# Performance work log

Measured on AMD Instinct MI355X. Metric: run time of the kernel, lower is better.

The kernel has to match this reference:

```python
import jax, jax.numpy as jnp
import numpy as np
import math

B = 50        # graphs per batch
NPG = 2000    # nodes per graph
EPG = 12000   # edges per graph
F_IN = 256
NHID = 128
RATIO = 0.8


def setup_inputs() -> dict:
    key = jax.random.key(0)
    ks = jax.random.split(key, 12)
    N = B * NPG
    src_loc = jax.random.randint(ks[0], (B, EPG), 0, NPG)
    dst_loc = jax.random.randint(ks[1], (B, EPG), 0, NPG)
    off = (jnp.arange(B) * NPG)[:, None]
    edge_index = jnp.stack([(src_loc + off).reshape(-1), (dst_loc + off).reshape(-1)]).astype(jnp.int32)

    def lin(k, fi, fo):
        return (jax.random.normal(k, (fi, fo), jnp.float32) / np.sqrt(fi).astype(np.float32))

    return {
        "x": jax.random.normal(ks[2], (N, F_IN), jnp.float32),
        "W1": lin(ks[3], F_IN, NHID), "b1": jnp.zeros(NHID, jnp.float32),
        "Ws1": lin(ks[4], NHID, 1), "bs1": jnp.zeros(1, jnp.float32),
        "W2": lin(ks[5], NHID, NHID), "b2": jnp.zeros(NHID, jnp.float32),
        "Ws2": lin(ks[6], NHID, 1), "bs2": jnp.zeros(1, jnp.float32),
        "W3": lin(ks[7], NHID, NHID), "b3": jnp.zeros(NHID, jnp.float32),
        "Ws3": lin(ks[8], NHID, 1), "bs3": jnp.zeros(1, jnp.float32),
        "Wl": lin(ks[9], 2 * NHID, NHID), "bl": jnp.zeros(NHID, jnp.float32),
        "edge_index": edge_index,
    }


def gcn_conv(x, W, b, src, dst, w, N):
    # PyG GCNConv: D^{-1/2} (A + I) D^{-1/2} X W + b, deg from edge weights + self loop
    h = x @ W
    deg = jax.ops.segment_sum(w, dst, num_segments=N) + 1.0
    dis = jax.lax.rsqrt(deg)
    norm = w * dis[src] * dis[dst]                       # [E]
    agg = jax.ops.segment_sum(h[src] * norm[:, None], dst, num_segments=N)
    return agg + h / deg[:, None] + b                    # self-loop norm = 1/deg


def sag_pool(x, src, dst, w, Ws, bs, n_per_graph):
    N = x.shape[0]
    k = math.ceil(RATIO * n_per_graph)
    score = gcn_conv(x, Ws, bs, src, dst, w, N)[:, 0]    # [N]
    _, topi = jax.lax.top_k(score.reshape(B, n_per_graph), k)
    perm = (topi + (jnp.arange(B) * n_per_graph)[:, None]).reshape(-1)
    x_new = x[perm] * jnp.tanh(score[perm])[:, None]
    # filter_adj: keep edges whose endpoints survive, reindex; dropped edges -> weight 0
    mapping = jnp.full((N,), -1, jnp.int32).at[perm].set(jnp.arange(B * k, dtype=jnp.int32))
    ns, nd = mapping[src], mapping[dst]
    valid = (ns >= 0) & (nd >= 0) & (w > 0)
    return (x_new, jnp.where(valid, ns, 0), jnp.where(valid, nd, 0),
            jnp.where(valid, w, jnp.zeros((), x.dtype)), k)


def readout(x, n):
    # global max pool || global mean pool (equal-size graphs, nodes grouped per graph)
    xr = x.reshape(B, n, -1)
    return jnp.concatenate([xr.max(axis=1), xr.mean(axis=1)], axis=-1)


def reference(x, W1, b1, Ws1, bs1, W2, b2, Ws2, bs2, W3, b3, Ws3, bs3, Wl, bl, edge_index):
    src, dst = edge_index[0], edge_index[1]
    w = jnp.ones(src.shape[0], x.dtype)
    n = NPG
    x = jax.nn.relu(gcn_conv(x, W1, b1, src, dst, w, B * n))
    x, src, dst, w, n = sag_pool(x, src, dst, w, Ws1, bs1, n)
    x1 = readout(x, n)
    x = jax.nn.relu(gcn_conv(x, W2, b2, src, dst, w, B * n))
    x, src, dst, w, n = sag_pool(x, src, dst, w, Ws2, bs2, n)
    x2 = readout(x, n)
    x = jax.nn.relu(gcn_conv(x, W3, b3, src, dst, w, B * n))
    x, src, dst, w, n = sag_pool(x, src, dst, w, Ws3, bs3, n)
    x3 = readout(x, n)
    return jax.nn.relu((x1 + x2 + x3) @ Wl + bl)
```

## Files before the change

### kernel.cpp

```cpp
#include <hip/hip_runtime.h>
#include <math.h>

#define B_GRAPHS 50
#define NPG0     2000
#define EPG      12000
#define F_IN_C   256
#define NHID     128
#define N0       (B_GRAPHS * NPG0)
#define NE       (B_GRAPHS * EPG)
#define RSEG     32
#define GSLOTS   7
#define CPAD     136
#define KMAX     1600

typedef _Float16 f16x8 __attribute__((ext_vector_type(8)));
typedef float    f32x4 __attribute__((ext_vector_type(4)));

static inline int cdiv(int a, int b) { return (a + b - 1) / b; }

__global__ void k_fill_start(int* __restrict__ cnt, float* __restrict__ accum) {
    int i = blockIdx.x * 256 + threadIdx.x;
    if (i < N0) cnt[i] = 0;
    if (i < B_GRAPHS * 256) accum[i] = 0.f;
}

__global__ void k_init_cvt(const int* __restrict__ ei, int* __restrict__ esrc,
                           int* __restrict__ edst, float* __restrict__ ew,
                           int* __restrict__ cnt,
                           const float* __restrict__ W1, const float* __restrict__ W2,
                           const float* __restrict__ W3, _Float16* __restrict__ WT1,
                           _Float16* __restrict__ WT2, _Float16* __restrict__ WT3) {
    int t = blockIdx.x * 256 + threadIdx.x;
    if (t < NE) {
        int d = ei[NE + t];
        esrc[t] = ei[t]; edst[t] = d; ew[t] = 1.0f;
        atomicAdd(&cnt[d], 1);
    }
    if (t < 128 * 256) {
        int n = t >> 8, kk = t & 255;
        WT1[t] = (_Float16)W1[kk * 128 + n];
    } else if (t < 128 * 256 + 128 * 128) {
        int u = t - 32768; int n = u >> 7, kk = u & 127;
        WT2[u] = (_Float16)W2[kk * 128 + n];
    } else if (t < 128 * 256 + 2 * 128 * 128) {
        int u = t - 49152; int n = u >> 7, kk = u & 127;
        WT3[u] = (_Float16)W3[kk * 128 + n];
    }
}

template<int FP32IN, int F, int GATHER>
__global__ __launch_bounds__(256) void k_gemm_ws(const void* __restrict__ Xin,
                                                 const _Float16* __restrict__ WT,
                                                 const int* __restrict__ perm,
                                                 const float* __restrict__ gate,
                                                 _Float16* __restrict__ H, int N) {
    constexpr int KH  = (F > 128) ? 128 : F;
    constexpr int K8H = KH / 8;
    constexpr int SMEMSZ = (128 * KH > 64 * CPAD) ? 128 * KH : 64 * CPAD;
    __shared__ _Float16 smem[SMEMSZ];
    const int tid  = threadIdx.x;
    const int wave = tid >> 6, lane = tid & 63;
    const int quad = lane >> 4, l16 = lane & 15;
    const int m_blk = blockIdx.x * 64;

    f32x4 acc[8];
#pragma unroll
    for (int j = 0; j < 8; ++j) acc[j] = {0.f, 0.f, 0.f, 0.f};

    int row0 = m_blk + wave * 16 + l16;
    if (row0 > N - 1) row0 = N - 1;
    _Float16 g0 = (_Float16)1.0f;
    if (GATHER) {
        g0 = (_Float16)gate[row0];
        row0 = perm[row0];
    }
    const int sx = l16 & 7;
    constexpr int NKQ = F / 32;

    if (FP32IN) {
        constexpr int PD = (NKQ < 4) ? NKQ : 4;
        const float* base0 = (const float*)Xin + (size_t)row0 * F + quad * 8;
        float4 p0[PD][2];
#pragma unroll
        for (int i = 0; i < PD; ++i) {
            p0[i][0] = ((const float4*)(base0 + i * 32))[0];
            p0[i][1] = ((const float4*)(base0 + i * 32))[1];
        }
#pragma unroll
        for (int c = tid; c < 128 * K8H; c += 256) {
            int n = c / K8H, k8 = c - n * K8H;
            f16x8 v = *(const f16x8*)&WT[(size_t)(n * (F / 8) + k8) * 8];
            *(f16x8*)&smem[n * KH + ((k8 ^ (n & 7)) << 3)] = v;
        }
        __syncthreads();
#pragma unroll
        for (int kq = 0; kq < NKQ; ++kq) {
            if (KH < F && kq == NKQ / 2) {
                __syncthreads();
#pragma unroll
                for (int c = tid; c < 128 * K8H; c += 256) {
                    int n = c / K8H, k8 = c - n * K8H;
                    f16x8 v = *(const f16x8*)&WT[(size_t)(n * (F / 8) + K8H + k8) * 8];
                    *(f16x8*)&smem[n * KH + ((k8 ^ (n & 7)) << 3)] = v;
                }
                __syncthreads();
            }
            const int b = kq % PD;
            float4 f0 = p0[b][0], f1 = p0[b][1];
            if (kq + PD < NKQ) {
                p0[b][0] = ((const float4*)(base0 + (kq + PD) * 32))[0];
                p0[b][1] = ((const float4*)(base0 + (kq + PD) * 32))[1];
            }
            f16x8 af0 = (f16x8){(_Float16)f0.x,(_Float16)f0.y,(_Float16)f0.z,(_Float16)f0.w,
                                (_Float16)f1.x,(_Float16)f1.y,(_Float16)f1.z,(_Float16)f1.w};
            f16x8 bf[8];
#pragma unroll
            for (int j = 0; j < 8; ++j)
                bf[j] = *(const f16x8*)&smem[(j * 16 + l16) * KH + (((((kq & 3) << 2) + quad) ^ sx) << 3)];
#pragma unroll
            for (int j = 0; j < 8; ++j)
                acc[j] = __builtin_amdgcn_mfma_f32_16x16x32_f16(af0, bf[j], acc[j], 0, 0, 0);
        }
    } else {
#pragma unroll
        for (int c = tid; c < 128 * K8H; c += 256) {
            int n = c / K8H, k8 = c - n * K8H;
            f16x8 v = *(const f16x8*)&WT[(size_t)(n * K8H + k8) * 8];
            *(f16x8*)&smem[n * KH + ((k8 ^ (n & 7)) << 3)] = v;
        }
        const _Float16* base0 = (const _Float16*)Xin + (size_t)row0 * F + quad * 8;
        f16x8 q0[NKQ];
#pragma unroll
        for (int i = 0; i < NKQ; ++i)
            q0[i] = *(const f16x8*)(base0 + i * 32);
        __syncthreads();
#pragma unroll
        for (int kq = 0; kq < NKQ; ++kq) {
            f16x8 af0 = q0[kq];
            if (GATHER) af0 = af0 * g0;
            f16x8 bf[8];
#pragma unroll
            for (int j = 0; j < 8; ++j)
                bf[j] = *(const f16x8*)&smem[(j * 16 + l16) * KH + (((((kq & 3) << 2) + quad) ^ sx) << 3)];
#pragma unroll
            for (int j = 0; j < 8; ++j)
                acc[j] = __builtin_amdgcn_mfma_f32_16x16x32_f16(af0, bf[j], acc[j], 0, 0, 0);
        }
    }
    __syncthreads();

    _Float16* sC = smem;
    const int rw = wave * 16;
#pragma unroll
    for (int j = 0; j < 8; ++j)
#pragma unroll
        for (int g = 0; g < 4; ++g)
            sC[(rw + quad * 4 + g) * CPAD + j * 16 + l16] = (_Float16)acc[j][g];
    __syncthreads();
    {
        int rr = tid >> 2;
        int cc = (tid & 3) * 32;
        int gr = m_blk + rr;
        if (gr < N) {
            _Float16* Hr = H + (size_t)gr * 128 + cc;
            const _Float16* Sr = sC + rr * CPAD + cc;
#pragma unroll
            for (int c = 0; c < 4; ++c)
                *(f16x8*)&Hr[c * 8] = *(const f16x8*)&Sr[c * 8];
        }
    }
}

__global__ __launch_bounds__(1024) void k_scancsr(const int* __restrict__ cnt,
                                                  int* __restrict__ offs,
                                                  const int* __restrict__ esrc,
                                                  const int* __restrict__ edst,
                                                  const float* __restrict__ ew,
                                                  int* __restrict__ csr_src,
                                                  float* __restrict__ csr_norm,
                                                  int npg) {
    __shared__ int ch[1024];
    __shared__ int scnt[2048];
    __shared__ int scur[2048];
    int b = blockIdx.x, tid = threadIdx.x;
    int base = b * npg;
    int per = (npg + 1023) >> 10;
    int s0 = tid * per;
    int s1 = s0 + per; if (s1 > npg) s1 = npg; if (s0 > npg) s0 = npg;
    int s = 0;
    for (int i = s0; i < s1; ++i) { int c = cnt[base + i]; scnt[i] = c; s += c; }
    ch[tid] = s;
    __syncthreads();
    for (int d = 1; d < 1024; d <<= 1) {
        int t = ch[tid] + ((tid >= d) ? ch[tid - d] : 0);
        __syncthreads();
        ch[tid] = t;
        __syncthreads();
    }
    int run = b * EPG + ch[tid] - s;
    for (int i = s0; i < s1; ++i) {
        offs[base + i] = run; scur[i] = run;
        run += scnt[i];
    }
    __syncthreads();
    int e0 = b * EPG;
    for (int e = tid; e < EPG; e += 1024) {
        float w = ew[e0 + e];
        if (w > 0.f) {
            int sN = esrc[e0 + e], d = edst[e0 + e];
            int pos = atomicAdd(&scur[d - base], 1);
            csr_src[pos] = sN;
            csr_norm[pos] = rsqrtf((float)(scnt[sN - base] + 1)) *
                            rsqrtf((float)(scnt[d - base] + 1));
        }
    }
}

__global__ __launch_bounds__(256) void k_agg(const _Float16* __restrict__ H,
                                             const int* __restrict__ csr_src,
                                             const float* __restrict__ csr_norm,
                                             const int* __restrict__ offs,
                                             const int* __restrict__ cnt,
                                             const float* __restrict__ bias,
                                             const float* __restrict__ Ws,
                                             _Float16* __restrict__ X,
                                             float* __restrict__ hs,
                                             int bpg, int npg) {
    int bi = blockIdx.x;
    int x = bi & 7, s = bi >> 3;
    int gslot = s / bpg, blk = s - gslot * bpg;
    int g = x + 8 * gslot;
    if (g >= B_GRAPHS) return;
    int node = g * npg + blk * 4 + (threadIdx.x >> 6);
    int lane = threadIdx.x & 63;
    int quad = lane >> 4, l16 = lane & 15;

    int st = offs[node], c = cnt[node], en = st + c;
    float acc[8];
#pragma unroll
    for (int j = 0; j < 8; ++j) acc[j] = 0.f;

    if (c > 0) {
        for (int e0 = st; e0 < en; e0 += 8) {
            int eA = e0 + quad, eB = eA + 4;
            int ecA = eA < en ? eA : en - 1;
            int ecB = eB < en ? eB : en - 1;
            int uA = csr_src[ecA], uB = csr_src[ecB];
            float nA = (eA < en) ? csr_norm[ecA] : 0.f;
            float nB = (eB < en) ? csr_norm[ecB] : 0.f;
            f16x8 hA = *(const f16x8*)&H[(size_t)uA * NHID + l16 * 8];
            f16x8 hB = *(const f16x8*)&H[(size_t)uB * NHID + l16 * 8];
#pragma unroll
            for (int j = 0; j < 8; ++j) acc[j] = fmaf((float)hA[j], nA, acc[j]);
#pragma unroll
            for (int j = 0; j < 8; ++j) acc[j] = fmaf((float)hB[j], nB, acc[j]);
        }
    }
#pragma unroll
    for (int j = 0; j < 8; ++j) {
        acc[j] += __shfl_xor(acc[j], 16, 64);
        acc[j] += __shfl_xor(acc[j], 32, 64);
    }
    float invd = 1.f / (float)(c + 1);
    f16x8 hn = *(const f16x8*)&H[(size_t)node * NHID + l16 * 8];
    float4 b0 = *(const float4*)&bias[l16 * 8];
    float4 b1 = *(const float4*)&bias[l16 * 8 + 4];
    float4 w0 = *(const float4*)&Ws[l16 * 8];
    float4 w1 = *(const float4*)&Ws[l16 * 8 + 4];
    const float bb[8] = {b0.x, b0.y, b0.z, b0.w, b1.x, b1.y, b1.z, b1.w};
    const float ww[8] = {w0.x, w0.y, w0.z, w0.w, w1.x, w1.y, w1.z, w1.w};
    float sd = 0.f;
    f16x8 o;
#pragma unroll
    for (int j = 0; j < 8; ++j) {
        float v = fmaxf(acc[j] + (float)hn[j] * invd + bb[j], 0.f);
        o[j] = (_Float16)v;
        sd = fmaf(v, ww[j], sd);
    }
    if (quad == 0)
        *(f16x8*)&X[(size_t)node * NHID + l16 * 8] = o;
    sd += __shfl_xor(sd, 1, 64);
    sd += __shfl_xor(sd, 2, 64);
    sd += __shfl_xor(sd, 4, 64);
    sd += __shfl_xor(sd, 8, 64);
    if (lane == 0) hs[node] = sd;
}

template<int REMAP>
__global__ __launch_bounds__(1024) void k_scoretopk(const float* __restrict__ hs,
                                                    const int* __restrict__ csr_src,
                                                    const float* __restrict__ csr_norm,
                                                    const int* __restrict__ offs,
                                                    const int* __restrict__ cnt,
                                                    const float* __restrict__ bs,
                                                    int* __restrict__ perm,
                                                    float* __restrict__ gate,
                                                    int* __restrict__ esrc,
                                                    int* __restrict__ edst,
                                                    float* __restrict__ ew,
                                                    int* __restrict__ cntN,
                                                    int npg, int k) {
    __shared__ float ss[2048];
    __shared__ int   si[2048];
    __shared__ float shs[2048];
    __shared__ int   shist[KMAX];
    int b = blockIdx.x, tid = threadIdx.x;
    int base = b * npg;
    float bs0 = bs[0];
    for (int i = tid; i < 2048; i += 1024)
        shs[i] = (i < npg) ? hs[base + i] : 0.f;
    __syncthreads();
    for (int i = tid; i < 2048; i += 1024) {
        if (i < npg) {
            int st = offs[base + i], c = cnt[base + i];
            float a = 0.f;
            for (int e = st; e < st + c; ++e)
                a = fmaf(shs[csr_src[e] - base], csr_norm[e], a);
            ss[i] = a + shs[i] / (float)(c + 1) + bs0;
        } else {
            ss[i] = -__builtin_inff();
        }
        si[i] = i;
    }
    __syncthreads();
    for (int size = 2; size <= 2048; size <<= 1) {
        for (int stride = size >> 1; stride > 0; stride >>= 1) {
            int t = tid;
            int i = ((t & ~(stride - 1)) << 1) | (t & (stride - 1));
            int j = i | stride;
            float sa = ss[i], sb = ss[j];
            int   ia = si[i], ib = si[j];
            bool b_before_a = (sb > sa) || (sb == sa && ib < ia);
            bool forward = ((i & size) == 0);
            bool doswap = forward ? b_before_a : !b_before_a;
            if (doswap) { ss[i] = sb; ss[j] = sa; si[i] = ib; si[j] = ia; }
            __syncthreads();
        }
    }
    int* smap = (int*)shs;
    for (int j = tid; j < npg; j += 1024) {
        int ol = si[j];
        if (j < k) {
            int newg = b * k + j;
            perm[newg] = base + ol;
            smap[ol] = newg;
            gate[newg] = tanhf(ss[j]);
        } else {
            smap[ol] = -1;
        }
    }
    if (REMAP) {
        for (int j = tid; j < k; j += 1024) shist[j] = 0;
        __syncthreads();
        int e0 = b * EPG;
        for (int e = tid; e < EPG; e += 1024) {
            int idx = e0 + e;
            float w = ew[idx];
            bool valid = false;
            int ns = 0, nd = 0;
            if (w > 0.f) {
                ns = smap[esrc[idx] - base];
                nd = smap[edst[idx] - base];
                valid = (ns >= 0) && (nd >= 0);
            }
            esrc[idx] = valid ? ns : 0;
            edst[idx] = valid ? nd : 0;
            ew[idx]   = valid ? w : 0.f;
            if (valid) atomicAdd(&shist[nd - b * k], 1);
        }
        __syncthreads();
        for (int j = tid; j < k; j += 1024) cntN[b * k + j] = shist[j];
    }
}

__global__ __launch_bounds__(128) void k_pool_readout(const _Float16* __restrict__ X,
                                                      const float* __restrict__ gate,
                                                      const int* __restrict__ perm,
                                                      float* __restrict__ pmax,
                                                      float* __restrict__ psum, int k) {
    int s = blockIdx.x, b = blockIdx.y, f = threadIdx.x;
    int j0 = (k * s) / RSEG, j1 = (k * (s + 1)) / RSEG;
    float mx = -__builtin_inff(), sm = 0.f;
    for (int j = j0; j < j1; ++j) {
        int g = b * k + j;
        int old = perm[g];
        float v = (float)X[(size_t)old * NHID + f] * gate[g];
        mx = fmaxf(mx, v);
        sm += v;
    }
    pmax[(size_t)(b * RSEG + s) * NHID + f] = mx;
    psum[(size_t)(b * RSEG + s) * NHID + f] = sm;
}

__global__ __launch_bounds__(128) void k_readout_comb(const float* __restrict__ pmax,
                                                      const float* __restrict__ psum,
                                                      float* __restrict__ accum, int k) {
    int b = blockIdx.x, f = threadIdx.x;
    float mx = -__builtin_inff(), sm = 0.f;
#pragma unroll
    for (int s = 0; s < RSEG; ++s) {
        mx = fmaxf(mx, pmax[(size_t)(b * RSEG + s) * NHID + f]);
        sm += psum[(size_t)(b * RSEG + s) * NHID + f];
    }
    accum[b * 256 + f]       += mx;
    accum[b * 256 + 128 + f] += sm / (float)k;
}

__global__ __launch_bounds__(128) void k_comb_final(const float* __restrict__ pmax,
                                                    const float* __restrict__ psum,
                                                    const float* __restrict__ accum,
                                                    const float* __restrict__ Wl,
                                                    const float* __restrict__ bl,
                                                    float* __restrict__ out, int k) {
    __shared__ float a[256];
    int b = blockIdx.x, f = threadIdx.x;
    float mx = -__builtin_inff(), sm = 0.f;
#pragma unroll
    for (int s = 0; s < RSEG; ++s) {
        mx = fmaxf(mx, pmax[(size_t)(b * RSEG + s) * NHID + f]);
        sm += psum[(size_t)(b * RSEG + s) * NHID + f];
    }
    a[f]       = accum[b * 256 + f] + mx;
    a[128 + f] = accum[b * 256 + 128 + f] + sm / (float)k;
    __syncthreads();
    float s = bl[f];
    for (int i = 0; i < 256; ++i) s = fmaf(a[i], Wl[i * NHID + f], s);
    out[b * NHID + f] = fmaxf(s, 0.f);
}

extern "C" void kernel_launch(void* const* d_in, const int* in_sizes, int n_in,
                              void* d_out, int out_size, void* d_ws, size_t ws_size,
                              hipStream_t stream) {
    const float* x0 = (const float*)d_in[0];
    const float* Wm[3] = {(const float*)d_in[1], (const float*)d_in[5], (const float*)d_in[9]};
    const float* bm[3] = {(const float*)d_in[2], (const float*)d_in[6], (const float*)d_in[10]};
    const float* Wsc[3] = {(const float*)d_in[3], (const float*)d_in[7], (const float*)d_in[11]};
    const float* bsc[3] = {(const float*)d_in[4], (const float*)d_in[8], (const float*)d_in[12]};
    const float* Wl = (const float*)d_in[13];
    const float* bl = (const float*)d_in[14];
    const int*   ei = (const int*)d_in[15];
    float* out = (float*)d_out;

    _Float16* bufA = (_Float16*)d_ws;
    _Float16* bufB = bufA + (size_t)N0 * NHID;
    _Float16* WT1  = bufB + (size_t)N0 * NHID;
    _Float16* WT2  = WT1 + 128 * 256;
    _Float16* WT3  = WT2 + 128 * 128;
    float* hs     = (float*)(WT3 + 128 * 128);
    float* gate   = hs + N0;
    float* accum  = gate + N0;
    float* pmax   = accum + B_GRAPHS * 256;
    float* psum   = pmax + B_GRAPHS * RSEG * NHID;
    int*   cntA   = (int*)(psum + B_GRAPHS * RSEG * NHID);
    int*   cntB   = cntA + N0;
    int*   offs   = cntB + N0;
    int*   perm   = offs + N0;
    int*   esrc   = perm + N0;
    int*   edst   = esrc + NE;
    float* ew     = (float*)(edst + NE);
    int*   csr_src= (int*)(ew + NE);
    float* csr_norm = (float*)(csr_src + NE);

    _Float16* WTs[3] = {WT1, WT2, WT3};
    const int EG = cdiv(NE, 256);

    k_fill_start<<<cdiv(N0, 256), 256, 0, stream>>>(cntA, accum);
    k_init_cvt<<<EG, 256, 0, stream>>>(ei, esrc, edst, ew, cntA,
                                       Wm[0], Wm[1], Wm[2], WT1, WT2, WT3);

    int npg = NPG0;
    _Float16* Hbuf = bufA; _Float16* Xbuf = bufB;

    for (int layer = 0; layer < 3; ++layer) {
        int N = B_GRAPHS * npg;
        int k = (npg * 4) / 5;
        int bpg = npg >> 2;
        int* cnt  = (layer == 1) ? cntB : cntA;
        int* cntN = (layer == 1) ? cntA : cntB;

        if (layer == 0)
            k_gemm_ws<1, 256, 0><<<cdiv(N, 64), 256, 0, stream>>>(x0, WTs[0], perm, gate, Hbuf, N);
        else
            k_gemm_ws<0, 128, 1><<<cdiv(N, 64), 256, 0, stream>>>(Xbuf, WTs[layer], perm, gate, Hbuf, N);
        k_scancsr<<<B_GRAPHS, 1024, 0, stream>>>(cnt, offs, esrc, edst, ew,
                                                 csr_src, csr_norm, npg);
        k_agg<<<8 * GSLOTS * bpg, 256, 0, stream>>>(Hbuf, csr_src, csr_norm, offs, cnt,
                                                    bm[layer], Wsc[layer], Xbuf, hs, bpg, npg);
        if (layer < 2) {
            k_scoretopk<1><<<B_GRAPHS, 1024, 0, stream>>>(hs, csr_src, csr_norm, offs, cnt,
                                                          bsc[layer], perm, gate,
                                                          esrc, edst, ew, cntN, npg, k);
        } else {
            k_scoretopk<0><<<B_GRAPHS, 1024, 0, stream>>>(hs, csr_src, csr_norm, offs, cnt,
                                                          bsc[layer], perm, gate,
                                                          esrc, edst, ew, cntN, npg, k);
        }
        k_pool_readout<<<dim3(RSEG, B_GRAPHS), 128, 0, stream>>>(Xbuf, gate, perm, pmax, psum, k);
        if (layer < 2) {
            k_readout_comb<<<B_GRAPHS, 128, 0, stream>>>(pmax, psum, accum, k);
        } else {
            k_comb_final<<<B_GRAPHS, 128, 0, stream>>>(pmax, psum, accum, Wl, bl, out, k);
        }

        npg = k;
    }
}
```

Measured before the change: 568.8 us.

## Fuse CSR rebuild and readout combine into score/top-k kernel

The score/top-k kernel now builds the next layer's CSR directly: it prefix-scans the per-node in-degree histogram, writes offsets and counts, and scatters source indices and normalization weights. This removes the separate k_scancsr launch for layers 1 and 2. It also takes over the previous layer's readout combine, so k_readout_comb is no longer launched. The work stays on only 50 blocks and uses atomic-position scatter, so edge order within each CSR segment is now nondeterministic.

New measurement: 549.6 us. 3.4% less time.

```diff
diff --git a/kernel.cpp b/kernel.cpp
--- a/kernel.cpp
+++ b/kernel.cpp
@@ -286,11 +286,11 @@
     if (lane == 0) hs[node] = sd;
 }
 
-template<int REMAP>
+template<int REMAP, int COMB>
 __global__ __launch_bounds__(1024) void k_scoretopk(const float* __restrict__ hs,
-                                                    const int* __restrict__ csr_src,
-                                                    const float* __restrict__ csr_norm,
-                                                    const int* __restrict__ offs,
+                                                    int* __restrict__ csr_src,
+                                                    float* __restrict__ csr_norm,
+                                                    int* __restrict__ offs,
                                                     const int* __restrict__ cnt,
                                                     const float* __restrict__ bs,
                                                     int* __restrict__ perm,
@@ -299,6 +299,9 @@
                                                     int* __restrict__ edst,
                                                     float* __restrict__ ew,
                                                     int* __restrict__ cntN,
+                                                    const float* __restrict__ pmax,
+                                                    const float* __restrict__ psum,
+                                                    float* __restrict__ accum,
                                                     int npg, int k) {
     __shared__ float ss[2048];
     __shared__ int   si[2048];
@@ -306,6 +309,21 @@
     __shared__ int   shist[KMAX];
     int b = blockIdx.x, tid = threadIdx.x;
     int base = b * npg;
+
+    if (COMB) {
+        if (tid < 2 * NHID) {
+            int f = tid & 127;
+            bool isSum = tid >= NHID;
+            float a2 = isSum ? 0.f : -__builtin_inff();
+            for (int s = 0; s < RSEG; ++s) {
+                float v = (isSum ? psum : pmax)[(size_t)(b * RSEG + s) * NHID + f];
+                a2 = isSum ? (a2 + v) : fmaxf(a2, v);
+            }
+            if (isSum) accum[b * 256 + 128 + f] += a2 / (float)npg;
+            else       accum[b * 256 + f]       += a2;
+        }
+    }
+
     float bs0 = bs[0];
     for (int i = tid; i < 2048; i += 1024)
         shs[i] = (i < npg) ? hs[base + i] : 0.f;
@@ -369,7 +387,39 @@
             if (valid) atomicAdd(&shist[nd - b * k], 1);
         }
         __syncthreads();
-        for (int j = tid; j < k; j += 1024) cntN[b * k + j] = shist[j];
+        int* sscan = (int*)ss;
+        int* scur  = si;
+        int per2 = (k + 1023) >> 10;
+        int t0 = tid * per2, t1 = t0 + per2;
+        if (t1 > k) t1 = k; if (t0 > k) t0 = k;
+        int sloc = 0;
+        for (int i = t0; i < t1; ++i) sloc += shist[i];
+        sscan[tid] = sloc;
+        __syncthreads();
+        for (int d = 1; d < 1024; d <<= 1) {
+            int t = sscan[tid] + ((tid >= d) ? sscan[tid - d] : 0);
+            __syncthreads();
+            sscan[tid] = t;
+            __syncthreads();
+        }
+        int run = b * EPG + sscan[tid] - sloc;
+        for (int i = t0; i < t1; ++i) {
+            offs[b * k + i] = run; scur[i] = run;
+            cntN[b * k + i] = shist[i];
+            run += shist[i];
+        }
+        __syncthreads();
+        for (int e = tid; e < EPG; e += 1024) {
+            int idx = e0 + e;
+            float w = ew[idx];
+            if (w > 0.f) {
+                int ns = esrc[idx], nd = edst[idx];
+                int pos = atomicAdd(&scur[nd - b * k], 1);
+                csr_src[pos] = ns;
+                csr_norm[pos] = rsqrtf((float)(shist[ns - b * k] + 1)) *
+                                rsqrtf((float)(shist[nd - b * k] + 1));
+            }
+        }
     }
 }
 
@@ -390,20 +440,6 @@
     }
     pmax[(size_t)(b * RSEG + s) * NHID + f] = mx;
     psum[(size_t)(b * RSEG + s) * NHID + f] = sm;
-}
-
-__global__ __launch_bounds__(128) void k_readout_comb(const float* __restrict__ pmax,
-                                                      const float* __restrict__ psum,
-                                                      float* __restrict__ accum, int k) {
-    int b = blockIdx.x, f = threadIdx.x;
-    float mx = -__builtin_inff(), sm = 0.f;
-#pragma unroll
-    for (int s = 0; s < RSEG; ++s) {
-        mx = fmaxf(mx, pmax[(size_t)(b * RSEG + s) * NHID + f]);
-        sm += psum[(size_t)(b * RSEG + s) * NHID + f];
-    }
-    accum[b * 256 + f]       += mx;
-    accum[b * 256 + 128 + f] += sm / (float)k;
 }
 
 __global__ __launch_bounds__(128) void k_comb_final(const float* __restrict__ pmax,
@@ -478,29 +514,33 @@
         int* cnt  = (layer == 1) ? cntB : cntA;
         int* cntN = (layer == 1) ? cntA : cntB;
 
-        if (layer == 0)
+        if (layer == 0) {
             k_gemm_ws<1, 256, 0><<<cdiv(N, 64), 256, 0, stream>>>(x0, WTs[0], perm, gate, Hbuf, N);
-        else
+            k_scancsr<<<B_GRAPHS, 1024, 0, stream>>>(cnt, offs, esrc, edst, ew,
+                                                     csr_src, csr_norm, npg);
+        } else {
             k_gemm_ws<0, 128, 1><<<cdiv(N, 64), 256, 0, stream>>>(Xbuf, WTs[layer], perm, gate, Hbuf, N);
-        k_scancsr<<<B_GRAPHS, 1024, 0, stream>>>(cnt, offs, esrc, edst, ew,
-                                                 csr_src, csr_norm, npg);
+        }
         k_agg<<<8 * GSLOTS * bpg, 256, 0, stream>>>(Hbuf, csr_src, csr_norm, offs, cnt,
                                                     bm[layer], Wsc[layer], Xbuf, hs, bpg, npg);
-        if (layer < 2) {
-            k_scoretopk<1><<<B_GRAPHS, 1024, 0, stream>>>(hs, csr_src, csr_norm, offs, cnt,
-                                                          bsc[layer], perm, gate,
-                                                          esrc, edst, ew, cntN, npg, k);
-        } else {
-            k_scoretopk<0><<<B_GRAPHS, 1024, 0, stream>>>(hs, csr_src, csr_norm, offs, cnt,
-                                                          bsc[layer], perm, gate,
-                                                          esrc, edst, ew, cntN, npg, k);
-        }
+        if (layer == 0)
+            k_scoretopk<1, 0><<<B_GRAPHS, 1024, 0, stream>>>(hs, csr_src, csr_norm, offs, cnt,
+                                                             bsc[layer], perm, gate,
+                                                             esrc, edst, ew, cntN,
+                                                             pmax, psum, accum, npg, k);
+        else if (layer == 1)
+            k_scoretopk<1, 1><<<B_GRAPHS, 1024, 0, stream>>>(hs, csr_src, csr_norm, offs, cnt,
+                                                             bsc[layer], perm, gate,
+                                                             esrc, edst, ew, cntN,
+                                                             pmax, psum, accum, npg, k);
+        else
+            k_scoretopk<0, 1><<<B_GRAPHS, 1024, 0, stream>>>(hs, csr_src, csr_norm, offs, cnt,
+                                                             bsc[layer], perm, gate,
+                                                             esrc, edst, ew, cntN,
+                                                             pmax, psum, accum, npg, k);
         k_pool_readout<<<dim3(RSEG, B_GRAPHS), 128, 0, stream>>>(Xbuf, gate, perm, pmax, psum, k);
-        if (layer < 2) {
-            k_readout_comb<<<B_GRAPHS, 128, 0, stream>>>(pmax, psum, accum, k);
-        } else {
+        if (layer == 2)
             k_comb_final<<<B_GRAPHS, 128, 0, stream>>>(pmax, psum, accum, Wl, bl, out, k);
-        }
 
         npg = k;
     }
```
